# Kernel optimization log

Measured on AMD Instinct MI355X. Metric: run time of the kernel, lower is better.

Reference implementation:

```python
import jax, jax.numpy as jnp
import numpy as np

K_BITS = 8
QMAX = float(2 ** (K_BITS - 1) - 1)  # 127 for symmetric int8 fake quant
BN_EPS = 1e-5
RES_SCALE = 1.0


def _ste(v, q):
    # straight-through estimator: forward q, backward identity wrt v
    return v + jax.lax.stop_gradient(q - v)


def quant_act(x, alpha):
    # PAMS-style: clamp to learnable alpha, symmetric uniform fake-quant
    xc = jnp.clip(x, -alpha, alpha)
    scale = alpha / QMAX
    q = jnp.round(xc / scale) * scale
    return _ste(xc, q)


def quant_weight(w):
    # symmetric max-abs weight fake-quant
    scale = jnp.max(jnp.abs(w)) / QMAX
    q = jnp.clip(jnp.round(w / scale), -QMAX, QMAX) * scale
    return _ste(w, q)


def conv3x3(x, w):
    return jax.lax.conv_general_dilated(
        x, w, window_strides=(1, 1), padding=[(1, 1), (1, 1)],
        dimension_numbers=("NCHW", "OIHW", "NCHW"))


def batchnorm(x, gamma, beta):
    # training-mode BN: biased batch statistics over (N, H, W)
    mean = jnp.mean(x, axis=(0, 2, 3), keepdims=True)
    var = jnp.var(x, axis=(0, 2, 3), keepdims=True)
    xhat = (x - mean) * jax.lax.rsqrt(var + BN_EPS)
    return xhat * gamma[None, :, None, None] + beta[None, :, None, None]


def prelu(x, a):
    return jnp.where(x >= 0, x, a * x)


def setup_inputs() -> dict:
    key = jax.random.key(0)
    ks = jax.random.split(key, 4)
    C = 64
    identity = jax.random.normal(ks[0], (8, C, 192, 192), dtype=jnp.float32)
    # conv weights, default_init_weights scale 0.1 (kaiming-ish * 0.1)
    w1 = jax.random.normal(ks[1], (C, C, 3, 3), dtype=jnp.float32) * 0.1
    w2 = jax.random.normal(ks[2], (C, C, 3, 3), dtype=jnp.float32) * 0.1
    return {
        "identity": identity,
        "bits": jnp.ones((1,), jnp.float32),
        "f": jnp.ones((1,), jnp.float32),
        "bits_out": jnp.zeros((1,), jnp.float32),
        "w1": w1,
        "w2": w2,
        "alpha1": jnp.array(8.0, jnp.float32),
        "alpha2": jnp.array(8.0, jnp.float32),
        "gamma1": jnp.ones((C,), jnp.float32),
        "beta1": jnp.zeros((C,), jnp.float32),
        "gamma2": jnp.ones((C,), jnp.float32),
        "beta2": jnp.zeros((C,), jnp.float32),
        "prelu_a": jnp.array(0.25, jnp.float32),
        "shortcut": jnp.ones((1,), jnp.float32),
    }


def reference(identity, bits, f, bits_out, w1, w2, alpha1, alpha2,
              gamma1, beta1, gamma2, beta2, prelu_a, shortcut):
    # quant conv1: quantize input act + weights, 3x3 conv
    x = conv3x3(quant_act(identity, alpha1), quant_weight(w1))
    # PReLU then BN1 (module applies bn1(act(x)))
    x = batchnorm(prelu(x, prelu_a), gamma1, beta1)
    # quant conv2
    out = conv3x3(quant_act(x, alpha2), quant_weight(w2))
    out = batchnorm(out, gamma2, beta2)
    out = identity * shortcut + out * RES_SCALE
    return (out, bits, f, bits_out)
```

## Files before the change

kernel.cpp:

```cpp
#include <hip/hip_runtime.h>
#include <hip/hip_bf16.h>
#include <math.h>

#define CNUM   64
#define HH     192
#define WW     192
#define NBATCH 8
#define HWSZ   (HH * WW)
#define CHWSZ  (CNUM * HWSZ)
#define TOTALSZ ((size_t)NBATCH * CHWSZ)
#define QMAXF  127.0f
#define BNEPS  1e-5f
#define PW     194
#define NPAD_SHORTS ((size_t)NBATCH * PW * PW * CNUM)
#define N_INT4  (NPAD_SHORTS / 8)

typedef __attribute__((ext_vector_type(8))) short bf16x8;
typedef __attribute__((ext_vector_type(4))) float f32x4;

#define OFF_PK1    0
#define OFF_PK2    18432
#define OFF_STATS  36864
#define OFF_SUM1   36864
#define OFF_SSQ1   37120
#define OFF_SUM2   37376
#define OFF_SSQ2   37632
#define OFF_WMAX   37888
#define OFF_SW     37890
#define OFF_AB1    37892
#define OFF_AB2    38020
#define OFF_QA     38148
#define OFF_QB     (38148 + 9634816)

__device__ inline void gload16(const void* g, void* l) {
    __builtin_amdgcn_global_load_lds(
        (const __attribute__((address_space(1))) unsigned int*)g,
        (__attribute__((address_space(3))) unsigned int*)l, 16, 0, 0);
}
__device__ inline float bf2f(unsigned short u) {
    return __builtin_bit_cast(float, (unsigned)u << 16);
}

__global__ __launch_bounds__(256)
void wmax_kernel(const float* __restrict__ w1,
                 const float* __restrict__ w2,
                 unsigned* __restrict__ wmaxbits) {
    const int which = blockIdx.y;
    const float4* w4 = (const float4*)(which ? w2 : w1);
    const int b = (blockIdx.x * 256 + threadIdx.x) * 2;
    const float4 a = w4[b], c = w4[b + 1];
    float m = fmaxf(fmaxf(fmaxf(fabsf(a.x), fabsf(a.y)), fmaxf(fabsf(a.z), fabsf(a.w))),
                    fmaxf(fmaxf(fabsf(c.x), fabsf(c.y)), fmaxf(fabsf(c.z), fabsf(c.w))));
#pragma unroll
    for (int off = 1; off < 64; off <<= 1) m = fmaxf(m, __shfl_xor(m, off));
    if ((threadIdx.x & 63) == 0)
        atomicMax(wmaxbits + which, __builtin_bit_cast(unsigned, m));
}

__global__ __launch_bounds__(256)
void wpack_kernel(const float* __restrict__ w1,
                  const float* __restrict__ w2,
                  const unsigned* __restrict__ wmaxbits,
                  short* __restrict__ pk1,
                  short* __restrict__ pk2,
                  float* __restrict__ swout) {
    const int which = blockIdx.y;
    const float* w  = which ? w2 : w1;
    short*       pk = which ? pk2 : pk1;
    const float scale = __builtin_bit_cast(float, wmaxbits[which]) / QMAXF;
    if (blockIdx.x == 0 && threadIdx.x == 0) swout[which] = scale;
    const int i0 = (blockIdx.x * 256 + threadIdx.x) * 8;
#pragma unroll
    for (int k = 0; k < 8; ++k) {
        const int i = i0 + k;
        const int j   = i & 7;
        const int l   = (i >> 3) & 63;
        const int ocb = (i >> 9) & 3;
        const int icb = (i >> 11) & 1;
        const int t   = i >> 12;
        const int oc  = ocb * 16 + (l & 15);
        const int ic  = icb * 32 + ((l >> 4) & 3) * 8 + j;
        float q = rintf(w[oc * 576 + ic * 9 + t] / scale);
        q = fminf(fmaxf(q, -QMAXF), QMAXF);
        pk[i] = (short)(__builtin_bit_cast(unsigned, q) >> 16);
    }
}

__global__ __launch_bounds__(256)
void requant_kernel(const float* __restrict__ inp,
                    const float* __restrict__ alpha_p,
                    short* __restrict__ q) {
    const int tid  = threadIdx.x;
    const int xblk = blockIdx.x;
    const int py   = blockIdx.y;
    const int n    = blockIdx.z;
    short* qrow = q + ((size_t)n * PW + py) * (PW * 64);

    if (py == 0 || py == PW - 1) {
        for (int i = xblk * 256 + tid; i < PW * 64 * 2 / 16; i += 768)
            ((int4*)qrow)[i] = make_int4(0, 0, 0, 0);
        return;
    }
    if (xblk == 0 && tid < 8) ((int4*)qrow)[tid] = make_int4(0, 0, 0, 0);
    if (xblk == 2 && tid < 8) ((int4*)(qrow + 193 * 64))[tid] = make_int4(0, 0, 0, 0);

    const int gy = py - 1;
    const int x0 = xblk * 64;
    const float alpha  = alpha_p[0];
    const float inv_qs = QMAXF / alpha;

    __shared__ short s[64 * 72];
    const int xq  = tid & 15;
    const int icl = tid >> 4;

    float4 r[4];
#pragma unroll
    for (int p = 0; p < 4; ++p) {
        const int ic = icl * 4 + p;
        const size_t fo = ((size_t)n * CNUM + ic) * HWSZ + (size_t)gy * WW + x0 + xq * 4;
        r[p] = *(const float4*)(inp + fo);
    }
#pragma unroll
    for (int p = 0; p < 4; ++p) {
        const int ic = icl * 4 + p;
        float vv[4] = {r[p].x, r[p].y, r[p].z, r[p].w};
#pragma unroll
        for (int j = 0; j < 4; ++j) {
            float v = fminf(fmaxf(vv[j], -alpha), alpha);
            v = rintf(v * inv_qs);
            s[(xq * 4 + j) * 72 + ic] = (short)(__builtin_bit_cast(unsigned, v) >> 16);
        }
    }
    __syncthreads();
#pragma unroll
    for (int h = 0; h < 2; ++h) {
        const int t    = h * 256 + tid;
        const int xx   = t >> 3;
        const int slot = t & 7;
        const int px   = 1 + xblk * 64 + xx;
        const int g    = slot ^ (px & 7);
        const int4 val = *(const int4*)&s[xx * 72 + g * 8];
        *(int4*)(qrow + (size_t)px * 64 + slot * 8) = val;
    }
}

__global__ __launch_bounds__(256)
void requant_inplace_kernel(short* __restrict__ qv,
                            const float* __restrict__ ab,
                            const float* __restrict__ alpha_p) {
    __shared__ float sab[128];
    if (threadIdx.x < 128) sab[threadIdx.x] = ab[threadIdx.x];
    __syncthreads();
    const unsigned i = blockIdx.x * 256 + threadIdx.x;
    const float alpha  = alpha_p[0];
    const float inv_qs = QMAXF / alpha;
    const unsigned t    = i >> 3;
    const unsigned slot = i & 7;
    const unsigned px   = t % 194u;
    const unsigned py   = (t / 194u) % 194u;
    int4 val = make_int4(0, 0, 0, 0);
    if ((px - 1u) < 192u && (py - 1u) < 192u) {
        const int g = (int)(slot ^ (px & 7u));
        const int4 v = ((const int4*)qv)[i];
        const unsigned short* u = (const unsigned short*)&v;
        unsigned w[4];
#pragma unroll
        for (int jj = 0; jj < 4; ++jj) {
            const int c0 = g * 8 + jj * 2;
            float x0 = sab[c0] * bf2f(u[jj * 2]) + sab[64 + c0];
            float x1 = sab[c0 + 1] * bf2f(u[jj * 2 + 1]) + sab[64 + c0 + 1];
            x0 = fminf(fmaxf(x0, -alpha), alpha);
            x1 = fminf(fmaxf(x1, -alpha), alpha);
            x0 = rintf(x0 * inv_qs);
            x1 = rintf(x1 * inv_qs);
            const unsigned b0 = __builtin_bit_cast(unsigned, x0);
            const unsigned b1 = __builtin_bit_cast(unsigned, x1);
            w[jj] = (b1 & 0xffff0000u) | (b0 >> 16);
        }
        val = make_int4((int)w[0], (int)w[1], (int)w[2], (int)w[3]);
    }
    ((int4*)qv)[i] = val;
}

__global__ __launch_bounds__(256, 3)
void conv_mfma_kernel(const short* __restrict__ q,
                      const short* __restrict__ wpk,
                      const float* __restrict__ swp,
                      const float* __restrict__ alpha_p,
                      const float* __restrict__ slope_p,
                      unsigned short* __restrict__ outp,
                      short* __restrict__ out_swz,
                      float* __restrict__ sum_g,
                      float* __restrict__ ssq_g) {
    __shared__ short s_in[6 * 66 * 64];
    __shared__ float sred[4 * 64], ssred[4 * 64];

    const int tid = threadIdx.x;
    const int x0 = blockIdx.x * 64;
    const int y0 = blockIdx.y * 4;
    const int n  = blockIdx.z;

    const short* g0 = q + ((size_t)(n * PW + y0) * PW + x0) * 64;
    for (int c = tid; c < 3168; c += 256) {
        const int r = c / 528;
        const int w = c - r * 528;
        gload16(g0 + (size_t)r * (PW * 64) + w * 8, &s_in[c * 8]);
    }
    __syncthreads();

    const int wave  = tid >> 6;
    const int lane  = tid & 63;
    const int xlane = lane & 15;
    const int icgl  = lane >> 4;

    f32x4 acc[4][4];
#pragma unroll
    for (int m = 0; m < 4; ++m)
#pragma unroll
        for (int nb = 0; nb < 4; ++nb) acc[m][nb] = (f32x4){0.f, 0.f, 0.f, 0.f};

#pragma unroll
    for (int t = 0; t < 9; ++t) {
        const int ky = t / 3, kx = t % 3;
        const int r = wave + ky;
#pragma unroll
        for (int icb = 0; icb < 2; ++icb) {
            const int icg = icb * 4 + icgl;
            bf16x8 bfrag[4], afrag[4];
            const short* bp = wpk + (size_t)((t * 2 + icb) * 4) * 512 + lane * 8;
#pragma unroll
            for (int nb = 0; nb < 4; ++nb) bfrag[nb] = *(const bf16x8*)(bp + nb * 512);
#pragma unroll
            for (int m = 0; m < 4; ++m) {
                const int x = m * 16 + xlane + kx;
                afrag[m] = *(const bf16x8*)&s_in[(size_t)((r * 66 + x) * 8 + (icg ^ (x & 7))) * 8];
            }
#pragma unroll
            for (int m = 0; m < 4; ++m)
#pragma unroll
                for (int nb = 0; nb < 4; ++nb)
                    acc[m][nb] = __builtin_amdgcn_mfma_f32_16x16x32_bf16(
                        afrag[m], bfrag[nb], acc[m][nb], 0, 0, 0);
        }
    }

    const float sfin  = (alpha_p[0] / QMAXF) * swp[0];
    const float slope = slope_p ? slope_p[0] : 1.0f;
    const int gy  = y0 + wave;
    const int gx0 = x0 + icgl * 4;

    if (out_swz) __syncthreads();
    short* sT = s_in + wave * (64 * 72);

#pragma unroll
    for (int nb = 0; nb < 4; ++nb) {
        const int oc = nb * 16 + xlane;
        float s = 0.0f, ss = 0.0f;
#pragma unroll
        for (int m = 0; m < 4; ++m) {
            float v[4];
#pragma unroll
            for (int rgi = 0; rgi < 4; ++rgi) {
                float a = acc[m][nb][rgi] * sfin;
                a = (a >= 0.0f) ? a : slope * a;
                v[rgi] = a;
                s += a;
                ss += a * a;
            }
            if (out_swz) {
#pragma unroll
                for (int rgi = 0; rgi < 4; ++rgi) {
                    const int pxl = m * 16 + icgl * 4 + rgi;
                    sT[pxl * 72 + oc] = (short)__builtin_bit_cast(
                        unsigned short, __float2bfloat16(v[rgi]));
                }
            } else {
                ushort4 pk;
                pk.x = __builtin_bit_cast(unsigned short, __float2bfloat16(v[0]));
                pk.y = __builtin_bit_cast(unsigned short, __float2bfloat16(v[1]));
                pk.z = __builtin_bit_cast(unsigned short, __float2bfloat16(v[2]));
                pk.w = __builtin_bit_cast(unsigned short, __float2bfloat16(v[3]));
                *(ushort4*)&outp[(size_t)(n * CNUM + oc) * HWSZ + (size_t)gy * WW + gx0 + m * 16] = pk;
            }
        }
        s  += __shfl_xor(s, 16);  s  += __shfl_xor(s, 32);
        ss += __shfl_xor(ss, 16); ss += __shfl_xor(ss, 32);
        if (icgl == 0) { sred[wave * 64 + oc] = s; ssred[wave * 64 + oc] = ss; }
    }

    if (out_swz) {
        const int py = gy + 1;
        short* qrow = out_swz + ((size_t)n * PW + py) * (PW * 64);
#pragma unroll
        for (int k = 0; k < 8; ++k) {
            const int idx  = k * 64 + lane;
            const int xx   = idx >> 3;
            const int slot = idx & 7;
            const int px   = x0 + 1 + xx;
            const int g    = slot ^ (px & 7);
            *(int4*)(qrow + (size_t)px * 64 + slot * 8) = *(const int4*)&sT[xx * 72 + g * 8];
        }
    }

    __syncthreads();
    const int bank = (blockIdx.y ^ blockIdx.z) & 3;
    if (tid < 64) {
        atomicAdd(sum_g + bank * 64 + tid,
                  sred[tid] + sred[64 + tid] + sred[128 + tid] + sred[192 + tid]);
    } else if (tid < 128) {
        const int c = tid - 64;
        atomicAdd(ssq_g + bank * 64 + c,
                  ssred[c] + ssred[64 + c] + ssred[128 + c] + ssred[192 + c]);
    }
}

__global__ void bnab_kernel(const float* __restrict__ sum,
                            const float* __restrict__ sumsq,
                            const float* __restrict__ gamma,
                            const float* __restrict__ beta,
                            float* __restrict__ ab) {
    const int c = threadIdx.x;
    const float cnt = (float)(NBATCH * HWSZ);
    const float sm = sum[c] + sum[64 + c] + sum[128 + c] + sum[192 + c];
    const float sq = sumsq[c] + sumsq[64 + c] + sumsq[128 + c] + sumsq[192 + c];
    const float mean = sm / cnt;
    const float var  = sq / cnt - mean * mean;
    const float inv  = 1.0f / sqrtf(var + BNEPS);
    const float a = gamma[c] * inv;
    ab[c] = a;
    ab[64 + c] = beta[c] - mean * a;
}

__global__ void final_kernel(const float* __restrict__ identity,
                             const unsigned short* __restrict__ t2,
                             const float* __restrict__ ab2,
                             const float* __restrict__ shortcut_p,
                             const float* __restrict__ bits,
                             const float* __restrict__ f,
                             const float* __restrict__ bits_out,
                             float* __restrict__ out) {
    const size_t i4 = (size_t)blockIdx.x * 256 + threadIdx.x;
    const float sc = shortcut_p[0];
    const int c = (int)((i4 / (HWSZ / 4)) % CNUM);
    const float a = ab2[c];
    const float b = ab2[64 + c];
    const float4 idv = ((const float4*)identity)[i4];
    const ushort4 tv = ((const ushort4*)t2)[i4];
    float4 o;
    o.x = idv.x * sc + a * bf2f(tv.x) + b;
    o.y = idv.y * sc + a * bf2f(tv.y) + b;
    o.z = idv.z * sc + a * bf2f(tv.z) + b;
    o.w = idv.w * sc + a * bf2f(tv.w) + b;
    ((float4*)out)[i4] = o;
    if (blockIdx.x == 0 && threadIdx.x == 0) {
        out[TOTALSZ + 0] = bits[0];
        out[TOTALSZ + 1] = f[0];
        out[TOTALSZ + 2] = bits_out[0];
    }
}

extern "C" void kernel_launch(void* const* d_in, const int* in_sizes, int n_in,
                              void* d_out, int out_size, void* d_ws, size_t ws_size,
                              hipStream_t stream) {
    const float* identity = (const float*)d_in[0];
    const float* bits     = (const float*)d_in[1];
    const float* f        = (const float*)d_in[2];
    const float* bits_out = (const float*)d_in[3];
    const float* w1       = (const float*)d_in[4];
    const float* w2       = (const float*)d_in[5];
    const float* alpha1   = (const float*)d_in[6];
    const float* alpha2   = (const float*)d_in[7];
    const float* gamma1   = (const float*)d_in[8];
    const float* beta1    = (const float*)d_in[9];
    const float* gamma2   = (const float*)d_in[10];
    const float* beta2    = (const float*)d_in[11];
    const float* prelu_a  = (const float*)d_in[12];
    const float* shortcut = (const float*)d_in[13];
    float* out = (float*)d_out;
    float* ws  = (float*)d_ws;

    short*    pk1   = (short*)(ws + OFF_PK1);
    short*    pk2   = (short*)(ws + OFF_PK2);
    float*    sum1  = ws + OFF_SUM1;
    float*    ssq1  = ws + OFF_SSQ1;
    float*    sum2  = ws + OFF_SUM2;
    float*    ssq2  = ws + OFF_SSQ2;
    unsigned* wmaxb = (unsigned*)(ws + OFF_WMAX);
    float*    sw    = ws + OFF_SW;
    float*    ab1   = ws + OFF_AB1;
    float*    ab2   = ws + OFF_AB2;
    short*          qa = (short*)(ws + OFF_QA);
    short*          qb = (short*)(ws + OFF_QB);
    unsigned short* t2 = (unsigned short*)(ws + OFF_QA);

    hipMemsetAsync(ws + OFF_STATS, 0, 1026 * sizeof(float), stream);
    hipLaunchKernelGGL(wmax_kernel, dim3(18, 2), dim3(256), 0, stream, w1, w2, wmaxb);
    hipLaunchKernelGGL(requant_kernel, dim3(3, PW, NBATCH), dim3(256), 0, stream,
                       identity, alpha1, qa);
    hipLaunchKernelGGL(wpack_kernel, dim3(18, 2), dim3(256), 0, stream,
                       w1, w2, wmaxb, pk1, pk2, sw);
    hipLaunchKernelGGL(conv_mfma_kernel, dim3(3, HH / 4, NBATCH), dim3(256), 0, stream,
                       qa, pk1, sw + 0, alpha1, prelu_a,
                       (unsigned short*)nullptr, qb, sum1, ssq1);
    hipLaunchKernelGGL(bnab_kernel, dim3(1), dim3(CNUM), 0, stream, sum1, ssq1, gamma1, beta1, ab1);
    hipLaunchKernelGGL(requant_inplace_kernel, dim3((unsigned)(N_INT4 / 256)), dim3(256), 0, stream,
                       qb, ab1, alpha2);
    hipLaunchKernelGGL(conv_mfma_kernel, dim3(3, HH / 4, NBATCH), dim3(256), 0, stream,
                       qb, pk2, sw + 1, alpha2, (const float*)nullptr,
                       t2, (short*)nullptr, sum2, ssq2);
    hipLaunchKernelGGL(bnab_kernel, dim3(1), dim3(CNUM), 0, stream, sum2, ssq2, gamma2, beta2, ab2);
    hipLaunchKernelGGL(final_kernel, dim3((unsigned)(TOTALSZ / 4 / 256)), dim3(256), 0, stream,
                       identity, t2, ab2, shortcut, bits, f, bits_out, out);
}
```

Before: 279.9 us.

## Fuse BN1 requant into conv2 tile load and fold BN coefficient kernels

Removes the separate in-place requantization pass over the padded intermediate. Conv2 now applies the BN1 affine, clamp and quantize while loading its input tile into LDS. Both bnab kernels are dropped: each conv2 and final block recomputes the per-channel scale and shift from the partial sums. The final kernel also processes four float4 per thread. The cost is that conv2 loses its asynchronous global-to-LDS loads, does redundant transform work on halo rows, and every block recomputes the BN coefficients.

```diff
diff --git a/kernel.cpp b/kernel.cpp
--- a/kernel.cpp
+++ b/kernel.cpp
@@ -12,8 +12,6 @@
 #define QMAXF  127.0f
 #define BNEPS  1e-5f
 #define PW     194
-#define NPAD_SHORTS ((size_t)NBATCH * PW * PW * CNUM)
-#define N_INT4  (NPAD_SHORTS / 8)
 
 typedef __attribute__((ext_vector_type(8))) short bf16x8;
 typedef __attribute__((ext_vector_type(4))) float f32x4;
@@ -27,8 +25,6 @@
 #define OFF_SSQ2   37632
 #define OFF_WMAX   37888
 #define OFF_SW     37890
-#define OFF_AB1    37892
-#define OFF_AB2    38020
 #define OFF_QA     38148
 #define OFF_QB     (38148 + 9634816)
 
@@ -144,67 +140,87 @@
     }
 }
 
-__global__ __launch_bounds__(256)
-void requant_inplace_kernel(short* __restrict__ qv,
-                            const float* __restrict__ ab,
-                            const float* __restrict__ alpha_p) {
-    __shared__ float sab[128];
-    if (threadIdx.x < 128) sab[threadIdx.x] = ab[threadIdx.x];
-    __syncthreads();
-    const unsigned i = blockIdx.x * 256 + threadIdx.x;
-    const float alpha  = alpha_p[0];
-    const float inv_qs = QMAXF / alpha;
-    const unsigned t    = i >> 3;
-    const unsigned slot = i & 7;
-    const unsigned px   = t % 194u;
-    const unsigned py   = (t / 194u) % 194u;
-    int4 val = make_int4(0, 0, 0, 0);
-    if ((px - 1u) < 192u && (py - 1u) < 192u) {
-        const int g = (int)(slot ^ (px & 7u));
-        const int4 v = ((const int4*)qv)[i];
-        const unsigned short* u = (const unsigned short*)&v;
-        unsigned w[4];
-#pragma unroll
-        for (int jj = 0; jj < 4; ++jj) {
-            const int c0 = g * 8 + jj * 2;
-            float x0 = sab[c0] * bf2f(u[jj * 2]) + sab[64 + c0];
-            float x1 = sab[c0 + 1] * bf2f(u[jj * 2 + 1]) + sab[64 + c0 + 1];
-            x0 = fminf(fmaxf(x0, -alpha), alpha);
-            x1 = fminf(fmaxf(x1, -alpha), alpha);
-            x0 = rintf(x0 * inv_qs);
-            x1 = rintf(x1 * inv_qs);
-            const unsigned b0 = __builtin_bit_cast(unsigned, x0);
-            const unsigned b1 = __builtin_bit_cast(unsigned, x1);
-            w[jj] = (b1 & 0xffff0000u) | (b0 >> 16);
-        }
-        val = make_int4((int)w[0], (int)w[1], (int)w[2], (int)w[3]);
-    }
-    ((int4*)qv)[i] = val;
-}
-
+template<int XFORM, int SWZOUT>
 __global__ __launch_bounds__(256, 3)
 void conv_mfma_kernel(const short* __restrict__ q,
                       const short* __restrict__ wpk,
                       const float* __restrict__ swp,
                       const float* __restrict__ alpha_p,
                       const float* __restrict__ slope_p,
+                      const float* __restrict__ st_sum,
+                      const float* __restrict__ st_ssq,
+                      const float* __restrict__ st_gamma,
+                      const float* __restrict__ st_beta,
                       unsigned short* __restrict__ outp,
                       short* __restrict__ out_swz,
                       float* __restrict__ sum_g,
                       float* __restrict__ ssq_g) {
     __shared__ short s_in[6 * 66 * 64];
     __shared__ float sred[4 * 64], ssred[4 * 64];
+    __shared__ float sab[128];
 
     const int tid = threadIdx.x;
     const int x0 = blockIdx.x * 64;
     const int y0 = blockIdx.y * 4;
     const int n  = blockIdx.z;
-
     const short* g0 = q + ((size_t)(n * PW + y0) * PW + x0) * 64;
-    for (int c = tid; c < 3168; c += 256) {
-        const int r = c / 528;
-        const int w = c - r * 528;
-        gload16(g0 + (size_t)r * (PW * 64) + w * 8, &s_in[c * 8]);
+
+    if (XFORM) {
+        if (tid < 64) {
+            const float cnt = (float)(NBATCH * HWSZ);
+            const float sm = st_sum[tid] + st_sum[64 + tid] + st_sum[128 + tid] + st_sum[192 + tid];
+            const float sq = st_ssq[tid] + st_ssq[64 + tid] + st_ssq[128 + tid] + st_ssq[192 + tid];
+            const float mean = sm / cnt;
+            const float var  = sq / cnt - mean * mean;
+            const float inv  = 1.0f / sqrtf(var + BNEPS);
+            const float a = st_gamma[tid] * inv;
+            sab[tid] = a;
+            sab[64 + tid] = st_beta[tid] - mean * a;
+        }
+        __syncthreads();
+        const float alpha  = alpha_p[0];
+        const float inv_qs = QMAXF / alpha;
+#pragma unroll
+        for (int k = 0; k < 13; ++k) {
+            const int c = tid + k * 256;
+            if (k == 12 && c >= 3168) break;
+            const int r  = c / 528;
+            const int w  = c - r * 528;
+            const int pxl = w >> 3, slot = w & 7;
+            const int px = x0 + pxl, py = y0 + r;
+            int4 val = make_int4(0, 0, 0, 0);
+            if ((unsigned)(px - 1) < 192u && (unsigned)(py - 1) < 192u) {
+                const int4 v = *(const int4*)(g0 + (size_t)r * (PW * 64) + w * 8);
+                const unsigned short* u = (const unsigned short*)&v;
+                const int gch = slot ^ (px & 7);
+                const float4 a0 = *(const float4*)&sab[gch * 8];
+                const float4 a1 = *(const float4*)&sab[gch * 8 + 4];
+                const float4 b0 = *(const float4*)&sab[64 + gch * 8];
+                const float4 b1 = *(const float4*)&sab[64 + gch * 8 + 4];
+                const float av[8] = {a0.x, a0.y, a0.z, a0.w, a1.x, a1.y, a1.z, a1.w};
+                const float bv[8] = {b0.x, b0.y, b0.z, b0.w, b1.x, b1.y, b1.z, b1.w};
+                unsigned wv[4];
+#pragma unroll
+                for (int jj = 0; jj < 4; ++jj) {
+                    float xx0 = av[jj * 2]     * bf2f(u[jj * 2])     + bv[jj * 2];
+                    float xx1 = av[jj * 2 + 1] * bf2f(u[jj * 2 + 1]) + bv[jj * 2 + 1];
+                    xx0 = fminf(fmaxf(xx0, -alpha), alpha);
+                    xx1 = fminf(fmaxf(xx1, -alpha), alpha);
+                    xx0 = rintf(xx0 * inv_qs);
+                    xx1 = rintf(xx1 * inv_qs);
+                    wv[jj] = (__builtin_bit_cast(unsigned, xx1) & 0xffff0000u) |
+                             (__builtin_bit_cast(unsigned, xx0) >> 16);
+                }
+                val = make_int4((int)wv[0], (int)wv[1], (int)wv[2], (int)wv[3]);
+            }
+            *(int4*)&s_in[c * 8] = val;
+        }
+    } else {
+        for (int c = tid; c < 3168; c += 256) {
+            const int r = c / 528;
+            const int w = c - r * 528;
+            gload16(g0 + (size_t)r * (PW * 64) + w * 8, &s_in[c * 8]);
+        }
     }
     __syncthreads();
 
@@ -249,7 +265,7 @@
     const int gy  = y0 + wave;
     const int gx0 = x0 + icgl * 4;
 
-    if (out_swz) __syncthreads();
+    if (SWZOUT) __syncthreads();
     short* sT = s_in + wave * (64 * 72);
 
 #pragma unroll
@@ -267,7 +283,7 @@
                 s += a;
                 ss += a * a;
             }
-            if (out_swz) {
+            if (SWZOUT) {
 #pragma unroll
                 for (int rgi = 0; rgi < 4; ++rgi) {
                     const int pxl = m * 16 + icgl * 4 + rgi;
@@ -288,7 +304,7 @@
         if (icgl == 0) { sred[wave * 64 + oc] = s; ssred[wave * 64 + oc] = ss; }
     }
 
-    if (out_swz) {
+    if (SWZOUT) {
         const int py = gy + 1;
         short* qrow = out_swz + ((size_t)n * PW + py) * (PW * 64);
 #pragma unroll
@@ -314,44 +330,57 @@
     }
 }
 
-__global__ void bnab_kernel(const float* __restrict__ sum,
-                            const float* __restrict__ sumsq,
-                            const float* __restrict__ gamma,
-                            const float* __restrict__ beta,
-                            float* __restrict__ ab) {
-    const int c = threadIdx.x;
-    const float cnt = (float)(NBATCH * HWSZ);
-    const float sm = sum[c] + sum[64 + c] + sum[128 + c] + sum[192 + c];
-    const float sq = sumsq[c] + sumsq[64 + c] + sumsq[128 + c] + sumsq[192 + c];
-    const float mean = sm / cnt;
-    const float var  = sq / cnt - mean * mean;
-    const float inv  = 1.0f / sqrtf(var + BNEPS);
-    const float a = gamma[c] * inv;
-    ab[c] = a;
-    ab[64 + c] = beta[c] - mean * a;
-}
-
-__global__ void final_kernel(const float* __restrict__ identity,
-                             const unsigned short* __restrict__ t2,
-                             const float* __restrict__ ab2,
-                             const float* __restrict__ shortcut_p,
-                             const float* __restrict__ bits,
-                             const float* __restrict__ f,
-                             const float* __restrict__ bits_out,
-                             float* __restrict__ out) {
-    const size_t i4 = (size_t)blockIdx.x * 256 + threadIdx.x;
+__global__ __launch_bounds__(256)
+void final_kernel(const float* __restrict__ identity,
+                  const unsigned short* __restrict__ t2,
+                  const float* __restrict__ st_sum,
+                  const float* __restrict__ st_ssq,
+                  const float* __restrict__ st_gamma,
+                  const float* __restrict__ st_beta,
+                  const float* __restrict__ shortcut_p,
+                  const float* __restrict__ bits,
+                  const float* __restrict__ f,
+                  const float* __restrict__ bits_out,
+                  float* __restrict__ out) {
+    __shared__ float sab[128];
+    if (threadIdx.x < 64) {
+        const int c = threadIdx.x;
+        const float cnt = (float)(NBATCH * HWSZ);
+        const float sm = st_sum[c] + st_sum[64 + c] + st_sum[128 + c] + st_sum[192 + c];
+        const float sq = st_ssq[c] + st_ssq[64 + c] + st_ssq[128 + c] + st_ssq[192 + c];
+        const float mean = sm / cnt;
+        const float var  = sq / cnt - mean * mean;
+        const float inv  = 1.0f / sqrtf(var + BNEPS);
+        const float a = st_gamma[c] * inv;
+        sab[c] = a;
+        sab[64 + c] = st_beta[c] - mean * a;
+    }
+    __syncthreads();
+
+    const size_t base = (size_t)blockIdx.x * 1024;
+    const int   cch  = (int)((base / (HWSZ / 4)) % CNUM);
+    const float a  = sab[cch];
+    const float bb = sab[64 + cch];
     const float sc = shortcut_p[0];
-    const int c = (int)((i4 / (HWSZ / 4)) % CNUM);
-    const float a = ab2[c];
-    const float b = ab2[64 + c];
-    const float4 idv = ((const float4*)identity)[i4];
-    const ushort4 tv = ((const ushort4*)t2)[i4];
-    float4 o;
-    o.x = idv.x * sc + a * bf2f(tv.x) + b;
-    o.y = idv.y * sc + a * bf2f(tv.y) + b;
-    o.z = idv.z * sc + a * bf2f(tv.z) + b;
-    o.w = idv.w * sc + a * bf2f(tv.w) + b;
-    ((float4*)out)[i4] = o;
+
+    float4  idv[4];
+    ushort4 tv[4];
+#pragma unroll
+    for (int k = 0; k < 4; ++k) {
+        const size_t i4 = base + (size_t)k * 256 + threadIdx.x;
+        idv[k] = ((const float4*)identity)[i4];
+        tv[k]  = ((const ushort4*)t2)[i4];
+    }
+#pragma unroll
+    for (int k = 0; k < 4; ++k) {
+        const size_t i4 = base + (size_t)k * 256 + threadIdx.x;
+        float4 o;
+        o.x = idv[k].x * sc + a * bf2f(tv[k].x) + bb;
+        o.y = idv[k].y * sc + a * bf2f(tv[k].y) + bb;
+        o.z = idv[k].z * sc + a * bf2f(tv[k].z) + bb;
+        o.w = idv[k].w * sc + a * bf2f(tv[k].w) + bb;
+        ((float4*)out)[i4] = o;
+    }
     if (blockIdx.x == 0 && threadIdx.x == 0) {
         out[TOTALSZ + 0] = bits[0];
         out[TOTALSZ + 1] = f[0];
@@ -387,8 +416,6 @@
     float*    ssq2  = ws + OFF_SSQ2;
     unsigned* wmaxb = (unsigned*)(ws + OFF_WMAX);
     float*    sw    = ws + OFF_SW;
-    float*    ab1   = ws + OFF_AB1;
-    float*    ab2   = ws + OFF_AB2;
     short*          qa = (short*)(ws + OFF_QA);
     short*          qb = (short*)(ws + OFF_QB);
     unsigned short* t2 = (unsigned short*)(ws + OFF_QA);
@@ -399,16 +426,16 @@
                        identity, alpha1, qa);
     hipLaunchKernelGGL(wpack_kernel, dim3(18, 2), dim3(256), 0, stream,
                        w1, w2, wmaxb, pk1, pk2, sw);
-    hipLaunchKernelGGL(conv_mfma_kernel, dim3(3, HH / 4, NBATCH), dim3(256), 0, stream,
+    hipLaunchKernelGGL((conv_mfma_kernel<0, 1>), dim3(3, HH / 4, NBATCH), dim3(256), 0, stream,
                        qa, pk1, sw + 0, alpha1, prelu_a,
+                       (const float*)nullptr, (const float*)nullptr,
+                       (const float*)nullptr, (const float*)nullptr,
                        (unsigned short*)nullptr, qb, sum1, ssq1);
-    hipLaunchKernelGGL(bnab_kernel, dim3(1), dim3(CNUM), 0, stream, sum1, ssq1, gamma1, beta1, ab1);
-    hipLaunchKernelGGL(requant_inplace_kernel, dim3((unsigned)(N_INT4 / 256)), dim3(256), 0, stream,
-                       qb, ab1, alpha2);
-    hipLaunchKernelGGL(conv_mfma_kernel, dim3(3, HH / 4, NBATCH), dim3(256), 0, stream,
+    hipLaunchKernelGGL((conv_mfma_kernel<1, 0>), dim3(3, HH / 4, NBATCH), dim3(256), 0, stream,
                        qb, pk2, sw + 1, alpha2, (const float*)nullptr,
+                       sum1, ssq1, gamma1, beta1,
                        t2, (short*)nullptr, sum2, ssq2);
-    hipLaunchKernelGGL(bnab_kernel, dim3(1), dim3(CNUM), 0, stream, sum2, ssq2, gamma2, beta2, ab2);
-    hipLaunchKernelGGL(final_kernel, dim3((unsigned)(TOTALSZ / 4 / 256)), dim3(256), 0, stream,
-                       identity, t2, ab2, shortcut, bits, f, bits_out, out);
-}
+    hipLaunchKernelGGL(final_kernel, dim3((unsigned)(TOTALSZ / 4 / 1024)), dim3(256), 0, stream,
+                       identity, t2, sum2, ssq2, gamma2, beta2,
+                       shortcut, bits, f, bits_out, out);
+}
```

New measurement: 268.0 us. 4.2% less time.
